# Kernel tuning notes

Hardware: AMD Instinct MI355X
Metric: run time of the kernel (lower is better)

## Reference

```python
import jax, jax.numpy as jnp
import numpy as np

B, S, D = 32, 200, 256          # batch, seq_len (hard-coded 200), emb_dim (hard-coded 256)
H_CLS, H_TNS, H = 2, 4, 6       # classical heads, tensor heads, total (rate=1/3, num_heads=6)
DFF, VOCAB, L, TD = 1024, 3500, 8, 2


def layer_norm(x, g, b, eps=1e-6):
    m = x.mean(-1, keepdims=True)
    v = ((x - m) ** 2).mean(-1, keepdims=True)
    return (x - m) * jax.lax.rsqrt(v + eps) * g + b


def setup_inputs() -> dict:
    key = jax.random.key(0)
    ks = jax.random.split(key, 12)
    n = jax.random.normal
    s1 = 1.0 / np.sqrt(4 + TD - 1.0)       # TNLayer RandomNormal stddev for A1/A4
    s2 = 1.0 / np.sqrt(4 + 2 * TD - 1.0)   # for A2/A3
    return {
        "tokens": jax.random.randint(ks[0], (B, S), 0, VOCAB),
        "tok_emb": n(ks[1], (VOCAB, D)) * 0.02,
        "pos_emb": n(ks[2], (S, D)) * 0.02,
        # stacked over L layers; axis 1 of size 3 is (q, k, v)
        "wqkv_w": n(ks[3], (L, 3, D, 2 * D)) * 0.05,
        "wqkv_b": jnp.zeros((L, 3, 2 * D)),
        "A1": n(ks[4], (L, 3, 4, TD, 4)) * s1,
        "A2": n(ks[5], (L, 3, 4, TD, TD, 8)) * s2,
        "A3": n(ks[6], (L, 3, 4, TD, TD, 8)) * s2,
        "A4": n(ks[7], (L, 3, 4, TD, 4)) * s1,
        "tnb": jnp.zeros((L, 3, 4 * D)),
        "out_w": n(ks[8], (L, H * D, D)) * 0.02,
        "out_b": jnp.zeros((L, D)),
        "ff1_w": n(ks[9], (L, D, DFF)) * 0.05,
        "ff1_b": jnp.zeros((L, DFF)),
        "ff2_w": n(ks[10], (L, DFF, D)) * 0.03,
        "ff2_b": jnp.zeros((L, D)),
        "ln1_g": jnp.ones((L, D)), "ln1_b": jnp.zeros((L, D)),
        "ln2_g": jnp.ones((L, D)), "ln2_b": jnp.zeros((L, D)),
    }


def bert_tensor_forward(tokens, tok_emb, pos_emb, wqkv_w, wqkv_b, A1, A2, A3, A4, tnb,
                        out_w, out_b, ff1_w, ff1_b, ff2_w, ff2_b, ln1_g, ln1_b, ln2_g, ln2_b):
    # embedding: positions array with start_index=1 is [0,1,...,199] -> pos_emb itself
    h = tok_emb[tokens] + pos_emb[None]                      # [B,S,D]
    # Attention_mask: 1.0 where token==0 (pad), broadcast over heads and query pos
    bias = (tokens == 0).astype(jnp.float32)[:, None, None, :] * (-1e9)  # [B,1,1,S]
    inv_sqrt_dk = 1.0 / jnp.sqrt(jnp.float32(D))

    def step(h, p):
        ww, wb, a1, a2, a3, a4, tb, ow, ob, f1w, f1b, f2w, f2b, g1, b1, g2, b2 = p
        # classical q/k/v heads: Dense(d_model * 2) -> [3,B,2,S,D]
        cls = jnp.einsum('bsd,xdf->xbsf', h, ww) + wb[:, None, None, :]
        cls = cls.reshape(3, B, S, H_CLS, D).transpose(0, 1, 3, 2, 4)
        # tensor-network q/k/v heads (TNLayer): MPO contraction over 4x4x4x4 split of D
        x6 = h.reshape(B, S, 4, 4, 4, 4)
        tns = jnp.einsum('bspqrt,xpmi,xqmnj,xrnok,xtol->xbsijkl', x6, a1, a2, a3, a4)
        tns = tns.reshape(3, B, S, 4 * D) + tb[:, None, None, :]
        tns = tns.reshape(3, B, S, H_TNS, D).transpose(0, 1, 3, 2, 4)  # [3,B,4,S,D]
        qkv = jnp.concatenate([cls, tns], axis=2)                      # [3,B,H,S,D]
        q, k, v = qkv[0], qkv[1], qkv[2]
        scores = jnp.einsum('bhqd,bhkd->bhqk', q, k) * inv_sqrt_dk + bias
        attn = jax.nn.softmax(scores, axis=-1)
        ctx = jnp.einsum('bhqk,bhkd->bhqd', attn, v)
        ctx = ctx.transpose(0, 2, 1, 3).reshape(B, S, H * D)           # [B,S,1536]
        out1 = layer_norm(h + ctx @ ow + ob, g1, b1)
        ffn = jax.nn.relu(out1 @ f1w + f1b) @ f2w + f2b
        return layer_norm(out1 + ffn, g2, b2), None

    xs = (wqkv_w, wqkv_b, A1, A2, A3, A4, tnb, out_w, out_b,
          ff1_w, ff1_b, ff2_w, ff2_b, ln1_g, ln1_b, ln2_g, ln2_b)
    h, _ = jax.lax.scan(step, h, xs)
    return h


def reference(tokens, tok_emb, pos_emb, wqkv_w, wqkv_b, A1, A2, A3, A4, tnb,
              out_w, out_b, ff1_w, ff1_b, ff2_w, ff2_b, ln1_g, ln1_b, ln2_g, ln2_b):
    return bert_tensor_forward(tokens, tok_emb, pos_emb, wqkv_w, wqkv_b, A1, A2, A3, A4,
                               tnb, out_w, out_b, ff1_w, ff1_b, ff2_w, ff2_b,
                               ln1_g, ln1_b, ln2_g, ln2_b)
```

## Files before the change

### kernel.cpp

```cpp
#include <hip/hip_runtime.h>
#include <hip/hip_bf16.h>

typedef __bf16 bf16x8 __attribute__((ext_vector_type(8)));
typedef float f32x4 __attribute__((ext_vector_type(4)));

#define NB 32
#define NS 200
#define SP 256
#define ND 256
#define NH 6
#define NL 8
#define NBS (NB*NS)
#define NZ (NB*NH)
#define SLAB (SP*ND)
#define PSTR 264

using bf16 = __hip_bfloat16;

enum { EPI_F32 = 0, EPI_RELU_BF = 1, EPI_QKV = 2, EPI_VT = 3 };

__device__ __forceinline__ float b2f(bf16 x) { return __bfloat162float(x); }
__device__ __forceinline__ bf16 f2b(float x) { return __float2bfloat16(x); }
__device__ __forceinline__ unsigned short fbits(float x) { bf16 h = f2b(x); return *(unsigned short*)&h; }

__device__ __forceinline__ void gload16(const bf16* g, const short* l) {
    __builtin_amdgcn_global_load_lds(
        (const __attribute__((address_space(1))) unsigned int*)(unsigned long long)(g),
        (__attribute__((address_space(3))) unsigned int*)(unsigned long long)(l), 16, 0, 0);
}

template<int MODE>
__global__ __launch_bounds__(256)
void gemm_nt(const bf16* __restrict__ A, const bf16* __restrict__ Bm,
             int M, int N, int K, int Kspan, long long sOz,
             float* __restrict__ outF, bf16* __restrict__ outBf,
             const float* __restrict__ bias,
             const float* __restrict__ qkvb, const float* __restrict__ tnbp,
             bf16* __restrict__ Qb, bf16* __restrict__ Kb, bf16* __restrict__ Vb)
{
    __shared__ short Asl[3][128*32];
    __shared__ short Bsl[3][128*32];
    const int tid  = threadIdx.x;
    const int m0   = blockIdx.y * 128;
    const int n0   = blockIdx.x * 128;
    const int kbase= blockIdx.z * Kspan;
    const int lane = tid & 63, w = tid >> 6;
    const int wm   = (w >> 1) * 64, wn = (w & 1) * 64;
    const int fr   = lane & 15, kc = (lane >> 4) * 8;
    const int srow = lane >> 2, schk = (lane & 3) * 8;

    const bf16* Ag = A  + (long long)m0 * K + kbase;
    const bf16* Bg = Bm + (long long)n0 * K + kbase;

    f32x4 acc[4][4];
#pragma unroll
    for (int i = 0; i < 4; i++)
#pragma unroll
        for (int j = 0; j < 4; j++) acc[i][j] = (f32x4){0.f,0.f,0.f,0.f};

    auto stage = [&](int buf, int k0) {
        gload16(Ag + (long long)(w*32      + srow)*K + k0 + schk, &Asl[buf][(w*32     )*32]);
        gload16(Ag + (long long)(w*32 + 16 + srow)*K + k0 + schk, &Asl[buf][(w*32 + 16)*32]);
        gload16(Bg + (long long)(w*32      + srow)*K + k0 + schk, &Bsl[buf][(w*32     )*32]);
        gload16(Bg + (long long)(w*32 + 16 + srow)*K + k0 + schk, &Bsl[buf][(w*32 + 16)*32]);
    };

    const int nt = Kspan >> 5;
    stage(0, 0);
    stage(1, 32);
    for (int t = 0; t < nt; t++) {
        const int buf = t % 3;
        if (t + 2 < nt) {
            stage((t + 2) % 3, (t + 2) * 32);
            asm volatile("s_waitcnt vmcnt(8)" ::: "memory");
        } else if (t + 1 < nt) {
            asm volatile("s_waitcnt vmcnt(4)" ::: "memory");
        } else {
            asm volatile("s_waitcnt vmcnt(0)" ::: "memory");
        }
        __builtin_amdgcn_s_barrier();
        __builtin_amdgcn_sched_barrier(0);
        bf16x8 af[4], bfm[4];
#pragma unroll
        for (int i = 0; i < 4; i++) af[i]  = *(const bf16x8*)&Asl[buf][(wm + i*16 + fr)*32 + kc];
#pragma unroll
        for (int j = 0; j < 4; j++) bfm[j] = *(const bf16x8*)&Bsl[buf][(wn + j*16 + fr)*32 + kc];
#pragma unroll
        for (int i = 0; i < 4; i++)
#pragma unroll
            for (int j = 0; j < 4; j++)
                acc[i][j] = __builtin_amdgcn_mfma_f32_16x16x32_bf16(af[i], bfm[j], acc[i][j], 0, 0, 0);
        __builtin_amdgcn_s_barrier();
        __builtin_amdgcn_sched_barrier(0);
    }

    const int rq = (lane >> 4) * 4;
#pragma unroll
    for (int i = 0; i < 4; i++) {
        const int r0 = m0 + wm + i*16 + rq;
        int b2r = 0, s20 = 0, hdV = 0, dd0 = 0;
        float bvv[4];
        if (MODE == EPI_QKV) { b2r = r0 / NS; s20 = r0 - b2r*NS; }
        if (MODE == EPI_VT) {
            hdV = r0 >> 8; dd0 = r0 & 255;
#pragma unroll
            for (int rg = 0; rg < 4; rg++) {
                const int rr = r0 + rg;
                bvv[rg] = (rr < 512) ? qkvb[1024 + rr] : tnbp[2048 + rr - 512];
            }
        }
#pragma unroll
        for (int j = 0; j < 4; j++) {
            const int c = n0 + wn + j*16 + fr;
            if (MODE == EPI_F32) {
#pragma unroll
                for (int rg = 0; rg < 4; rg++)
                    outF[(long long)blockIdx.z * sOz + (long long)(r0+rg)*N + c] = acc[i][j][rg];
            } else if (MODE == EPI_RELU_BF) {
                const float bv = bias[c];
#pragma unroll
                for (int rg = 0; rg < 4; rg++)
                    outBf[(long long)(r0+rg)*N + c] = f2b(fmaxf(acc[i][j][rg] + bv, 0.f));
            } else if (MODE == EPI_QKV) {
                const int x  = (c >= 1536);
                const int c1 = c - x*1536;
                const int hd = c1 >> 8, dd = c1 & 255;
                const float bv = (c1 < 512) ? qkvb[x*512 + c1] : tnbp[x*1024 + (c1 - 512)];
                bf16* dst = x ? Kb : Qb;
#pragma unroll
                for (int rg = 0; rg < 4; rg++) {
                    int bb = b2r, ss = s20 + rg;
                    if (ss >= NS) { bb++; ss -= NS; }
                    dst[((long long)((bb*NH + hd)*SP + ss))*ND + dd] = f2b(acc[i][j][rg] + bv);
                }
            } else {
                const int b2 = c / NS;
                const int s2 = c - b2*NS;
                const long long base = ((long long)((b2*NH + hdV)*ND + dd0))*SP + s2;
#pragma unroll
                for (int rg = 0; rg < 4; rg++)
                    Vb[base + (long long)rg*SP] = f2b(acc[i][j][rg] + bvv[rg]);
            }
        }
    }
}

__global__ __launch_bounds__(256)
void attn_fused(const bf16* __restrict__ Qb, const bf16* __restrict__ Kb,
                const bf16* __restrict__ Vtb, const int* __restrict__ tokens,
                bf16* __restrict__ ctx)
{
    __shared__ __align__(16) char smem[16384 + 4096 + 1024 + 1024 + 64*PSTR*2];
    short* Ks    = (short*)smem;
    short* Qs    = (short*)(smem + 16384);
    float* red   = (float*)(smem + 16384 + 4096);
    float* maskv = (float*)(smem + 16384 + 4096 + 1024);
    short* P     = (short*)(smem + 16384 + 4096 + 2048);

    const int z = blockIdx.y;
    const int b = z / NH, h = z - b*NH;
    const int q0 = blockIdx.x * 64;
    const int tid = threadIdx.x;
    const int lane = tid & 63, w = tid >> 6;
    const int fr = lane & 15, qh = lane >> 4;
    const int kc = qh * 8;
    const int srow = lane >> 2, schk = (lane & 3) * 8;

    const bf16* Kp = Kb  + (long long)z * SLAB;
    const bf16* Qp = Qb  + (long long)z * SLAB;
    const bf16* Vp = Vtb + (long long)z * SLAB;

    {
        const int s = tid;
        float mv = -1e9f;
        if (s < NS && tokens[b*NS + s] != 0) mv = 0.f;
        maskv[s] = mv;
    }

    f32x4 acc[4][4];
#pragma unroll
    for (int i = 0; i < 4; i++)
#pragma unroll
        for (int j = 0; j < 4; j++) acc[i][j] = (f32x4){0.f,0.f,0.f,0.f};

    for (int k0 = 0; k0 < ND; k0 += 32) {
#pragma unroll
        for (int r2 = 0; r2 < 4; r2++)
            gload16(Kp + (long long)(w*64 + r2*16 + srow)*ND + k0 + schk, &Ks[(w*64 + r2*16)*32]);
        gload16(Qp + (long long)(q0 + w*16 + srow)*ND + k0 + schk, &Qs[(w*16)*32]);
        __syncthreads();
        bf16x8 ak[4], bq[4];
#pragma unroll
        for (int i = 0; i < 4; i++) ak[i] = *(const bf16x8*)&Ks[(w*64 + i*16 + fr)*32 + kc];
#pragma unroll
        for (int j = 0; j < 4; j++) bq[j] = *(const bf16x8*)&Qs[(j*16 + fr)*32 + kc];
#pragma unroll
        for (int i = 0; i < 4; i++)
#pragma unroll
            for (int j = 0; j < 4; j++)
                acc[i][j] = __builtin_amdgcn_mfma_f32_16x16x32_bf16(ak[i], bq[j], acc[i][j], 0, 0, 0);
        __syncthreads();
    }

    float mk[4][4];
#pragma unroll
    for (int i = 0; i < 4; i++)
#pragma unroll
        for (int rg = 0; rg < 4; rg++) mk[i][rg] = maskv[w*64 + i*16 + qh*4 + rg];
#pragma unroll
    for (int i = 0; i < 4; i++)
#pragma unroll
        for (int j = 0; j < 4; j++)
#pragma unroll
            for (int rg = 0; rg < 4; rg++)
                acc[i][j][rg] = acc[i][j][rg] * 0.0625f + mk[i][rg];

    float pm[4];
#pragma unroll
    for (int j = 0; j < 4; j++) {
        float m = -3.0e38f;
#pragma unroll
        for (int i = 0; i < 4; i++)
#pragma unroll
            for (int rg = 0; rg < 4; rg++) m = fmaxf(m, acc[i][j][rg]);
        m = fmaxf(m, __shfl_xor(m, 16));
        m = fmaxf(m, __shfl_xor(m, 32));
        pm[j] = m;
    }
#pragma unroll
    for (int j = 0; j < 4; j++) red[w*64 + j*16 + fr] = pm[j];
    __syncthreads();
    float gm[4];
#pragma unroll
    for (int j = 0; j < 4; j++)
        gm[j] = fmaxf(fmaxf(red[j*16 + fr], red[64 + j*16 + fr]),
                      fmaxf(red[128 + j*16 + fr], red[192 + j*16 + fr]));
    float ps[4] = {0.f, 0.f, 0.f, 0.f};
#pragma unroll
    for (int i = 0; i < 4; i++)
#pragma unroll
        for (int j = 0; j < 4; j++)
#pragma unroll
            for (int rg = 0; rg < 4; rg++) {
                float e = __expf(acc[i][j][rg] - gm[j]);
                acc[i][j][rg] = e;
                ps[j] += e;
            }
#pragma unroll
    for (int j = 0; j < 4; j++) {
        ps[j] += __shfl_xor(ps[j], 16);
        ps[j] += __shfl_xor(ps[j], 32);
    }
    __syncthreads();
#pragma unroll
    for (int j = 0; j < 4; j++) red[w*64 + j*16 + fr] = ps[j];
    __syncthreads();
    float inv[4];
#pragma unroll
    for (int j = 0; j < 4; j++)
        inv[j] = 1.f / (red[j*16 + fr] + red[64 + j*16 + fr] + red[128 + j*16 + fr] + red[192 + j*16 + fr]);

#pragma unroll
    for (int i = 0; i < 4; i++)
#pragma unroll
        for (int j = 0; j < 4; j++) {
            ushort4 pk;
            pk.x = fbits(acc[i][j][0] * inv[j]);
            pk.y = fbits(acc[i][j][1] * inv[j]);
            pk.z = fbits(acc[i][j][2] * inv[j]);
            pk.w = fbits(acc[i][j][3] * inv[j]);
            *(ushort4*)&P[(j*16 + fr)*PSTR + w*64 + i*16 + qh*4] = pk;
        }

    f32x4 acc2[4][4];
#pragma unroll
    for (int i = 0; i < 4; i++)
#pragma unroll
        for (int j = 0; j < 4; j++) acc2[i][j] = (f32x4){0.f,0.f,0.f,0.f};

    for (int s0 = 0; s0 < 224; s0 += 32) {
#pragma unroll
        for (int r2 = 0; r2 < 4; r2++)
            gload16(Vp + (long long)(w*64 + r2*16 + srow)*SP + s0 + schk, &Ks[(w*64 + r2*16)*32]);
        __syncthreads();
        bf16x8 ap[4], bv[4];
#pragma unroll
        for (int i = 0; i < 4; i++) ap[i] = *(const bf16x8*)&P[(i*16 + fr)*PSTR + s0 + kc];
#pragma unroll
        for (int j = 0; j < 4; j++) bv[j] = *(const bf16x8*)&Ks[(w*64 + j*16 + fr)*32 + kc];
#pragma unroll
        for (int i = 0; i < 4; i++)
#pragma unroll
            for (int j = 0; j < 4; j++)
                acc2[i][j] = __builtin_amdgcn_mfma_f32_16x16x32_bf16(ap[i], bv[j], acc2[i][j], 0, 0, 0);
        __syncthreads();
    }

#pragma unroll
    for (int i = 0; i < 4; i++)
#pragma unroll
        for (int j = 0; j < 4; j++)
#pragma unroll
            for (int rg = 0; rg < 4; rg++) {
                const int qg = q0 + i*16 + qh*4 + rg;
                if (qg < NS) {
                    const int d = w*64 + j*16 + fr;
                    ctx[((long long)(b*NS + qg))*1536 + h*256 + d] = f2b(acc2[i][j][rg]);
                }
            }
}

__global__ void embed_kernel(const int* __restrict__ tokens, const float* __restrict__ tok_emb,
                             const float* __restrict__ pos_emb, float* __restrict__ hf,
                             bf16* __restrict__ hbf)
{
    long long id = (long long)blockIdx.x * 256 + threadIdx.x;
    if (id >= (long long)NBS * ND) return;
    long long r = id >> 8;
    int j = id & 255;
    int tk = tokens[r];
    int s  = (int)(r % NS);
    float v = tok_emb[(long long)tk * ND + j] + pos_emb[s * ND + j];
    hf[id]  = v;
    hbf[id] = f2b(v);
}

__global__ void transpose_w(const float* __restrict__ in, bf16* __restrict__ out,
                            int L, int R, int C, long long total)
{
    long long id = (long long)blockIdx.x * 256 + threadIdx.x;
    if (id >= total) return;
    int l = (int)(id / ((long long)R * C));
    long long rem = id - (long long)l * R * C;
    int c = (int)(rem / R);
    int r = (int)(rem - (long long)c * R);
    out[id] = f2b(in[((long long)l * R + r) * C + c]);
}

__global__ void pack_cls(const float* __restrict__ wqkv, bf16* __restrict__ wcat)
{
    long long id = (long long)blockIdx.x * 256 + threadIdx.x;
    if (id >= 24ll * 512 * 256) return;
    int lx = (int)(id / (512 * 256));
    int rem = (int)(id - (long long)lx * 512 * 256);
    int n = rem >> 8;
    int k = rem & 255;
    wcat[((long long)lx * 1536 + n) * 256 + k] = f2b(wqkv[((long long)lx * 256 + k) * 512 + n]);
}

__global__ __launch_bounds__(256)
void build_wtns(const float* __restrict__ A1, const float* __restrict__ A2,
                const float* __restrict__ A3, const float* __restrict__ A4,
                bf16* __restrict__ wcat)
{
    int lx = blockIdx.x;
    __shared__ float a1s[32], a2s[128], a3s[128], a4s[32];
    int t = threadIdx.x;
    if (t < 32)  { a1s[t] = A1[lx*32 + t]; a4s[t] = A4[lx*32 + t]; }
    if (t < 128) { a2s[t] = A2[lx*128 + t]; a3s[t] = A3[lx*128 + t]; }
    __syncthreads();
    int d = t;
    int p = d >> 6, q = (d >> 4) & 3, rr = (d >> 2) & 3, tt = d & 3;
    for (int i = 0; i < 4; i++) {
        float w1_0 = a1s[(p*2 + 0)*4 + i];
        float w1_1 = a1s[(p*2 + 1)*4 + i];
        for (int j = 0; j < 8; j++) {
            float c1_0 = w1_0 * a2s[((q*2+0)*2+0)*8 + j] + w1_1 * a2s[((q*2+1)*2+0)*8 + j];
            float c1_1 = w1_0 * a2s[((q*2+0)*2+1)*8 + j] + w1_1 * a2s[((q*2+1)*2+1)*8 + j];
            for (int kk = 0; kk < 8; kk++) {
                float c2_0 = c1_0 * a3s[((rr*2+0)*2+0)*8 + kk] + c1_1 * a3s[((rr*2+1)*2+0)*8 + kk];
                float c2_1 = c1_0 * a3s[((rr*2+0)*2+1)*8 + kk] + c1_1 * a3s[((rr*2+1)*2+1)*8 + kk];
                for (int ll = 0; ll < 4; ll++) {
                    float sv = c2_0 * a4s[(tt*2 + 0)*4 + ll] + c2_1 * a4s[(tt*2 + 1)*4 + ll];
                    int e = ((i*8 + j)*8 + kk)*4 + ll;
                    wcat[((long long)lx * 1536 + 512 + e) * 256 + d] = f2b(sv);
                }
            }
        }
    }
}

__global__ __launch_bounds__(256)
void ln_kernel(const float* __restrict__ raw0, const float* __restrict__ raw1,
               const float* __restrict__ bias, const float* __restrict__ resid,
               const float* __restrict__ g, const float* __restrict__ bb,
               float* __restrict__ outF, bf16* __restrict__ outBf)
{
    int w = threadIdx.x >> 6, lane = threadIdx.x & 63;
    long long r = (long long)blockIdx.x * 4 + w;
    long long base = r * ND;
    float x[4]; float s = 0.f;
#pragma unroll
    for (int c = 0; c < 4; c++) {
        int j = lane + 64*c;
        x[c] = resid[base + j] + raw0[base + j] + raw1[base + j] + bias[j];
        s += x[c];
    }
#pragma unroll
    for (int o = 32; o; o >>= 1) s += __shfl_xor(s, o);
    float mean = s * (1.f/256.f);
    float vs = 0.f;
#pragma unroll
    for (int c = 0; c < 4; c++) { float d = x[c] - mean; vs += d*d; }
#pragma unroll
    for (int o = 32; o; o >>= 1) vs += __shfl_xor(vs, o);
    float rs = rsqrtf(vs * (1.f/256.f) + 1e-6f);
#pragma unroll
    for (int c = 0; c < 4; c++) {
        int j = lane + 64*c;
        float y = (x[c] - mean) * rs * g[j] + bb[j];
        outF[base + j]  = y;
        outBf[base + j] = f2b(y);
    }
}

extern "C" void kernel_launch(void* const* d_in, const int* in_sizes, int n_in,
                              void* d_out, int out_size, void* d_ws, size_t ws_size,
                              hipStream_t stream)
{
    const int*   tokens  = (const int*)  d_in[0];
    const float* tok_emb = (const float*)d_in[1];
    const float* pos_emb = (const float*)d_in[2];
    const float* wqkv_w  = (const float*)d_in[3];
    const float* wqkv_b  = (const float*)d_in[4];
    const float* A1      = (const float*)d_in[5];
    const float* A2      = (const float*)d_in[6];
    const float* A3      = (const float*)d_in[7];
    const float* A4      = (const float*)d_in[8];
    const float* tnb     = (const float*)d_in[9];
    const float* out_w   = (const float*)d_in[10];
    const float* out_b   = (const float*)d_in[11];
    const float* ff1_w   = (const float*)d_in[12];
    const float* ff1_b   = (const float*)d_in[13];
    const float* ff2_w   = (const float*)d_in[14];
    const float* ff2_b   = (const float*)d_in[15];
    const float* ln1_g   = (const float*)d_in[16];
    const float* ln1_b   = (const float*)d_in[17];
    const float* ln2_g   = (const float*)d_in[18];
    const float* ln2_b   = (const float*)d_in[19];

    char* ws = (char*)d_ws;
    size_t off = 0;
    auto alloc = [&](size_t bytes) -> char* {
        char* p = ws + off;
        off += (bytes + 255) & ~(size_t)255;
        return p;
    };
    float* hf    = (float*)alloc((size_t)NBS * ND * 4);
    bf16*  hbf   = (bf16*) alloc((size_t)NBS * ND * 2);
    bf16*  wcat  = (bf16*) alloc(24ull * 1536 * 256 * 2);
    bf16*  owt   = (bf16*) alloc(8ull * 256 * 1536 * 2);
    bf16*  f1wt  = (bf16*) alloc(8ull * 1024 * 256 * 2);
    bf16*  f2wt  = (bf16*) alloc(8ull * 256 * 1024 * 2);
    bf16*  Qb    = (bf16*) alloc((size_t)NZ * SLAB * 2);
    bf16*  Kb    = (bf16*) alloc((size_t)NZ * SLAB * 2);
    bf16*  Vtb   = (bf16*) alloc((size_t)NZ * SLAB * 2);
    bf16*  ctxg  = (bf16*) alloc((size_t)NBS * 1536 * 2);
    bf16*  ffn   = (bf16*) alloc((size_t)NBS * 1024 * 2);
    float* raw   = (float*)alloc((size_t)NBS * ND * 4 * 2);
    float* out1f = (float*)alloc((size_t)NBS * ND * 4);
    bf16*  out1bf= (bf16*) alloc((size_t)NBS * ND * 2);
    if (off > ws_size) return;
    float* raw1 = raw + (size_t)NBS * ND;

    hipMemsetAsync(Qb,  0, (size_t)NZ * SLAB * 2, stream);
    hipMemsetAsync(Kb,  0, (size_t)NZ * SLAB * 2, stream);
    hipMemsetAsync(Vtb, 0, (size_t)NZ * SLAB * 2, stream);

    embed_kernel<<<NBS, 256, 0, stream>>>(tokens, tok_emb, pos_emb, hf, hbf);
    pack_cls<<<12288, 256, 0, stream>>>(wqkv_w, wcat);
    build_wtns<<<24, 256, 0, stream>>>(A1, A2, A3, A4, wcat);
    transpose_w<<<12288, 256, 0, stream>>>(out_w, owt, 8, 1536, 256, 8ll*1536*256);
    transpose_w<<<8192, 256, 0, stream>>>(ff1_w, f1wt, 8, 256, 1024, 8ll*256*1024);
    transpose_w<<<8192, 256, 0, stream>>>(ff2_w, f2wt, 8, 1024, 256, 8ll*1024*256);

    for (int l = 0; l < NL; l++) {
        const bf16* wl = wcat + (long long)l * 3 * 1536 * 256;
        gemm_nt<EPI_QKV><<<dim3(24, 50, 1), 256, 0, stream>>>(
            hbf, wl, NBS, 3072, 256, 256, 0, nullptr, nullptr, nullptr,
            wqkv_b + l * 3 * 512, tnb + l * 3 * 1024, Qb, Kb, nullptr);
        gemm_nt<EPI_VT><<<dim3(50, 12, 1), 256, 0, stream>>>(
            wl + 2ll * 1536 * 256, hbf, 1536, NBS, 256, 256, 0, nullptr, nullptr, nullptr,
            wqkv_b + l * 3 * 512, tnb + l * 3 * 1024, nullptr, nullptr, Vtb);
        attn_fused<<<dim3(4, NZ), 256, 0, stream>>>(Qb, Kb, Vtb, tokens, ctxg);
        gemm_nt<EPI_F32><<<dim3(2, 50, 2), 256, 0, stream>>>(
            ctxg, owt + (long long)l * 256 * 1536, NBS, 256, 1536, 768, (long long)NBS*ND,
            raw, nullptr, nullptr, nullptr, nullptr, nullptr, nullptr, nullptr);
        ln_kernel<<<1600, 256, 0, stream>>>(raw, raw1, out_b + l * 256, hf,
                                            ln1_g + l * 256, ln1_b + l * 256, out1f, out1bf);
        gemm_nt<EPI_RELU_BF><<<dim3(8, 50, 1), 256, 0, stream>>>(
            out1bf, f1wt + (long long)l * 1024 * 256, NBS, 1024, 256, 256, 0,
            nullptr, ffn, ff1_b + l * 1024, nullptr, nullptr, nullptr, nullptr, nullptr);
        gemm_nt<EPI_F32><<<dim3(2, 50, 2), 256, 0, stream>>>(
            ffn, f2wt + (long long)l * 256 * 1024, NBS, 256, 1024, 512, (long long)NBS*ND,
            raw, nullptr, nullptr, nullptr, nullptr, nullptr, nullptr, nullptr);
        ln_kernel<<<1600, 256, 0, stream>>>(raw, raw1, ff2_b + l * 256, out1f,
                                            ln2_g + l * 256, ln2_b + l * 256,
                                            (l == NL - 1) ? (float*)d_out : hf, hbf);
    }
}
```

Baseline: 1.147 ms.

## Double-buffer K/Q and V tile loads in fused attention kernel

```diff
diff --git a/kernel.cpp b/kernel.cpp
--- a/kernel.cpp
+++ b/kernel.cpp
@@ -150,16 +150,14 @@
                 const bf16* __restrict__ Vtb, const int* __restrict__ tokens,
                 bf16* __restrict__ ctx)
 {
-    __shared__ __align__(16) char smem[16384 + 4096 + 1024 + 1024 + 64*PSTR*2];
-    short* Ks    = (short*)smem;
-    short* Qs    = (short*)(smem + 16384);
-    float* red   = (float*)(smem + 16384 + 4096);
-    float* maskv = (float*)(smem + 16384 + 4096 + 1024);
-    short* P     = (short*)(smem + 16384 + 4096 + 2048);
-
-    const int z = blockIdx.y;
-    const int b = z / NH, h = z - b*NH;
-    const int q0 = blockIdx.x * 64;
+    __shared__ __align__(16) char smem[2*20480 + 1024 + 1024 + 64*PSTR*2];
+    float* red   = (float*)(smem + 40960);
+    float* maskv = (float*)(smem + 40960 + 1024);
+    short* P     = (short*)(smem + 40960 + 2048);
+
+    const int z  = blockIdx.x;
+    const int b  = z / NH, h = z - b*NH;
+    const int q0 = blockIdx.y * 64;
     const int tid = threadIdx.x;
     const int lane = tid & 63, w = tid >> 6;
     const int fr = lane & 15, qh = lane >> 4;
@@ -177,18 +175,34 @@
         maskv[s] = mv;
     }
 
-    f32x4 acc[4][4];
-#pragma unroll
-    for (int i = 0; i < 4; i++)
-#pragma unroll
-        for (int j = 0; j < 4; j++) acc[i][j] = (f32x4){0.f,0.f,0.f,0.f};
-
-    for (int k0 = 0; k0 < ND; k0 += 32) {
+    auto stage1 = [&](int buf, int k0) {
+        short* Ks = (short*)(smem + buf*20480);
+        short* Qs = (short*)(smem + buf*20480 + 16384);
 #pragma unroll
         for (int r2 = 0; r2 < 4; r2++)
             gload16(Kp + (long long)(w*64 + r2*16 + srow)*ND + k0 + schk, &Ks[(w*64 + r2*16)*32]);
         gload16(Qp + (long long)(q0 + w*16 + srow)*ND + k0 + schk, &Qs[(w*16)*32]);
-        __syncthreads();
+    };
+
+    f32x4 acc[4][4];
+#pragma unroll
+    for (int i = 0; i < 4; i++)
+#pragma unroll
+        for (int j = 0; j < 4; j++) acc[i][j] = (f32x4){0.f,0.f,0.f,0.f};
+
+    stage1(0, 0);
+    for (int t = 0; t < 8; t++) {
+        const int buf = t & 1;
+        if (t + 1 < 8) {
+            stage1(buf ^ 1, (t + 1) * 32);
+            asm volatile("s_waitcnt vmcnt(5)" ::: "memory");
+        } else {
+            asm volatile("s_waitcnt vmcnt(0)" ::: "memory");
+        }
+        __builtin_amdgcn_s_barrier();
+        __builtin_amdgcn_sched_barrier(0);
+        const short* Ks = (const short*)(smem + buf*20480);
+        const short* Qs = (const short*)(smem + buf*20480 + 16384);
         bf16x8 ak[4], bq[4];
 #pragma unroll
         for (int i = 0; i < 4; i++) ak[i] = *(const bf16x8*)&Ks[(w*64 + i*16 + fr)*32 + kc];
@@ -199,7 +213,8 @@
 #pragma unroll
             for (int j = 0; j < 4; j++)
                 acc[i][j] = __builtin_amdgcn_mfma_f32_16x16x32_bf16(ak[i], bq[j], acc[i][j], 0, 0, 0);
-        __syncthreads();
+        __builtin_amdgcn_s_barrier();
+        __builtin_amdgcn_sched_barrier(0);
     }
 
     float mk[4][4];
@@ -271,6 +286,14 @@
             pk.w = fbits(acc[i][j][3] * inv[j]);
             *(ushort4*)&P[(j*16 + fr)*PSTR + w*64 + i*16 + qh*4] = pk;
         }
+    __syncthreads();
+
+    auto stage2 = [&](int buf, int s0) {
+        short* Vs = (short*)(smem + buf*20480);
+#pragma unroll
+        for (int r2 = 0; r2 < 4; r2++)
+            gload16(Vp + (long long)(w*64 + r2*16 + srow)*SP + s0 + schk, &Vs[(w*64 + r2*16)*32]);
+    };
 
     f32x4 acc2[4][4];
 #pragma unroll
@@ -278,22 +301,30 @@
 #pragma unroll
         for (int j = 0; j < 4; j++) acc2[i][j] = (f32x4){0.f,0.f,0.f,0.f};
 
-    for (int s0 = 0; s0 < 224; s0 += 32) {
-#pragma unroll
-        for (int r2 = 0; r2 < 4; r2++)
-            gload16(Vp + (long long)(w*64 + r2*16 + srow)*SP + s0 + schk, &Ks[(w*64 + r2*16)*32]);
-        __syncthreads();
+    stage2(0, 0);
+    for (int t = 0; t < 7; t++) {
+        const int buf = t & 1;
+        if (t + 1 < 7) {
+            stage2(buf ^ 1, (t + 1) * 32);
+            asm volatile("s_waitcnt vmcnt(4)" ::: "memory");
+        } else {
+            asm volatile("s_waitcnt vmcnt(0)" ::: "memory");
+        }
+        __builtin_amdgcn_s_barrier();
+        __builtin_amdgcn_sched_barrier(0);
+        const short* Vs = (const short*)(smem + buf*20480);
         bf16x8 ap[4], bv[4];
 #pragma unroll
-        for (int i = 0; i < 4; i++) ap[i] = *(const bf16x8*)&P[(i*16 + fr)*PSTR + s0 + kc];
-#pragma unroll
-        for (int j = 0; j < 4; j++) bv[j] = *(const bf16x8*)&Ks[(w*64 + j*16 + fr)*32 + kc];
+        for (int i = 0; i < 4; i++) ap[i] = *(const bf16x8*)&P[(i*16 + fr)*PSTR + t*32 + kc];
+#pragma unroll
+        for (int j = 0; j < 4; j++) bv[j] = *(const bf16x8*)&Vs[(w*64 + j*16 + fr)*32 + kc];
 #pragma unroll
         for (int i = 0; i < 4; i++)
 #pragma unroll
             for (int j = 0; j < 4; j++)
                 acc2[i][j] = __builtin_amdgcn_mfma_f32_16x16x32_bf16(ap[i], bv[j], acc2[i][j], 0, 0, 0);
-        __syncthreads();
+        __builtin_amdgcn_s_barrier();
+        __builtin_amdgcn_sched_barrier(0);
     }
 
 #pragma unroll
@@ -482,7 +513,7 @@
         gemm_nt<EPI_VT><<<dim3(50, 12, 1), 256, 0, stream>>>(
             wl + 2ll * 1536 * 256, hbf, 1536, NBS, 256, 256, 0, nullptr, nullptr, nullptr,
             wqkv_b + l * 3 * 512, tnb + l * 3 * 1024, nullptr, nullptr, Vtb);
-        attn_fused<<<dim3(4, NZ), 256, 0, stream>>>(Qb, Kb, Vtb, tokens, ctxg);
+        attn_fused<<<dim3(NZ, 4), 256, 0, stream>>>(Qb, Kb, Vtb, tokens, ctxg);
         gemm_nt<EPI_F32><<<dim3(2, 50, 2), 256, 0, stream>>>(
             ctxg, owt + (long long)l * 256 * 1536, NBS, 256, 1536, 768, (long long)NBS*ND,
             raw, nullptr, nullptr, nullptr, nullptr, nullptr, nullptr, nullptr);
```

Measured after the change: 1.046 ms. 8.8% less time.
